# Kernel optimization log

Hardware: AMD Instinct MI355X
Metric: run time of the kernel (lower is better)

Reference implementation:

```python
import jax, jax.numpy as jnp
import numpy as np

# SRM neuron constants (match init_kwargs)
THRESH = 0.3
TAU_M = 16.0
TAU_S = 4.0
DT = 1.0
LENS = 0.5
DECAY_M = float(np.exp(-DT / TAU_M))
DECAY_S = float(np.exp(-DT / TAU_S))

B, T = 16, 16
SHAPES = [(B, 64, 64, 64), (B, 128, 64, 64), (B, 128, 32, 32), (B, 512), (B, 11)]


@jax.custom_vjp
def spike_fn(u):
    # Heaviside spike with rectangular surrogate gradient (width 2*lens),
    # the smooth-math stand-in for the LUT-based grad_u_approx.
    return (u > THRESH).astype(u.dtype)

def _spike_fwd(u):
    return spike_fn(u), u

def _spike_bwd(u, g):
    surr = (jnp.abs(u - THRESH) < LENS).astype(u.dtype) / (2.0 * LENS)
    return (g * surr,)

spike_fn.defvjp(_spike_fwd, _spike_bwd)


def conv(x, w):
    # 3x3 conv, stride 1, padding 1, no bias (NCHW / OIHW)
    return jax.lax.conv_general_dilated(x, w, (1, 1), [(1, 1), (1, 1)],
                                        dimension_numbers=('NCHW', 'OIHW', 'NCHW'))


def maxpool2(x):
    return jax.lax.reduce_window(x, -jnp.inf, jax.lax.max, (1, 1, 2, 2), (1, 1, 2, 2), 'VALID')


def srm_update(I, vm, vs, s_prev):
    # SRM dynamics: two exponential traces (LUT exp decay in original),
    # reset via previous spike, membrane potential u = vm - vs.
    vm = DECAY_M * vm * (1.0 - s_prev) + I
    vs = DECAY_S * vs * (1.0 - s_prev) + I
    s = spike_fn(vm - vs)
    return vm, vs, s


def _xavier(key, shape):
    if len(shape) == 4:  # OIHW conv
        fan_in = shape[1] * shape[2] * shape[3]
        fan_out = shape[0] * shape[2] * shape[3]
    else:  # Linear [out, in]
        fan_in, fan_out = shape[1], shape[0]
    lim = float(np.sqrt(6.0 / (fan_in + fan_out)))
    return jax.random.uniform(key, shape, jnp.float32, -lim, lim)


def setup_inputs() -> dict:
    key = jax.random.key(0)
    ks = jax.random.split(key, 6)
    inp = jax.random.uniform(ks[0], (B, T, 2, 64, 64), jnp.float32)
    return {
        'input': inp,
        'W0': _xavier(ks[1], (64, 2, 3, 3)),
        'W1': _xavier(ks[2], (128, 64, 3, 3)),
        'W2': _xavier(ks[3], (128, 128, 3, 3)),
        'W3': _xavier(ks[4], (512, 32768)),
        'W4': _xavier(ks[5], (11, 512)),
        'batch_size': B,
        'num_steps': T,
    }


def reference(input, W0, W1, W2, W3, W4, batch_size, num_steps):
    x = jnp.transpose(input, (1, 0, 2, 3, 4))  # [T, B, 2, 64, 64]
    z = lambda s: jnp.zeros(s, jnp.float32)
    vm = tuple(z(s) for s in SHAPES)
    vs = tuple(z(s) for s in SHAPES)
    sp = tuple(z(s) for s in SHAPES)
    out_sum = z((batch_size, 11))

    def step(carry, xt):
        vm, vs, sp, out_sum = carry
        in_spike = jnp.clip(xt, 0.0, 1.0)  # limit == 'yes'
        vm0, vs0, s0 = srm_update(conv(in_spike, W0), vm[0], vs[0], sp[0])
        vm1, vs1, s1 = srm_update(conv(s0, W1), vm[1], vs[1], sp[1])
        p1 = maxpool2(s1)                                    # [B,128,32,32]
        vm2, vs2, s2 = srm_update(conv(p1, W2), vm[2], vs[2], sp[2])
        p2 = maxpool2(s2).reshape(batch_size, -1)            # [B, 32768]
        vm3, vs3, s3 = srm_update(p2 @ W3.T, vm[3], vs[3], sp[3])
        vm4, vs4, s4 = srm_update(s3 @ W4.T, vm[4], vs[4], sp[4])
        new_carry = ((vm0, vm1, vm2, vm3, vm4), (vs0, vs1, vs2, vs3, vs4),
                     (s0, s1, s2, s3, s4), out_sum + s4)
        return new_carry, None

    (_, _, _, out_sum), _ = jax.lax.scan(step, (vm, vs, sp, out_sum), x)
    return out_sum / num_steps
```

## Files before the change

kernel.cpp:

```cpp
#include <hip/hip_runtime.h>
#include <hip/hip_bf16.h>
#include <math.h>

#define DM 0.9394130628134758f
#define DSC 0.7788007830714049f
#define TH 0.3f

#define B 16
#define T 16

typedef short short8 __attribute__((ext_vector_type(8)));
typedef float f32x4 __attribute__((ext_vector_type(4)));
typedef int i32x4 __attribute__((ext_vector_type(4)));

__device__ __forceinline__ void srm(float& m, float& s, float p, float I, float& spk) {
    m = DM * m * (1.f - p) + I;
    s = DSC * s * (1.f - p) + I;
    spk = (m - s > TH) ? 1.f : 0.f;
}

__global__ __launch_bounds__(256) void k_prep_i8(const float* __restrict__ W,
                                                 signed char* __restrict__ Wd,
                                                 int CO, int CI,
                                                 float s1, float s2, float s3) {
    int idx = blockIdx.x * 256 + threadIdx.x;
    int total = CO * CI * 9;
    if (idx >= total) return;
    int tap = idx % 9, tmp = idx / 9, ci = tmp % CI, co = tmp / CI;
    float w = W[((size_t)co * CI + ci) * 9 + tap];
    float d1 = rintf(w / s1);
    float r1 = fmaf(-d1, s1, w);
    float d2 = rintf(r1 / s2);
    float r2 = fmaf(-d2, s2, r1);
    float d3 = rintf(r2 / s3);
    d1 = fminf(fmaxf(d1, -127.f), 127.f);
    d2 = fminf(fmaxf(d2, -127.f), 127.f);
    d3 = fminf(fmaxf(d3, -127.f), 127.f);
    size_t base = ((size_t)tap * CO + co) * CI + ci;
    size_t stride = (size_t)9 * CO * CI;
    Wd[base] = (signed char)(int)d1;
    Wd[base + stride] = (signed char)(int)d2;
    Wd[base + 2 * stride] = (signed char)(int)d3;
}

__global__ __launch_bounds__(256) void k_prep3(const float* __restrict__ W3,
                                               unsigned short* __restrict__ W3p) {
    int bid = blockIdx.x;
    int ot = bid >> 8, ks4 = bid & 255;
    int lane = threadIdx.x & 63, wv = threadIdx.x >> 6;
    int kstep = ks4 * 4 + wv;
    int n = lane & 15, q = lane >> 4;
    const float* src = W3 + (size_t)(ot * 16 + n) * 32768 + kstep * 32 + q * 8;
    float4 w0 = *(const float4*)src;
    float4 w1 = *(const float4*)(src + 4);
    float wj[8] = {w0.x, w0.y, w0.z, w0.w, w1.x, w1.y, w1.z, w1.w};
    short8 hh, mm, ll;
#pragma unroll
    for (int j = 0; j < 8; j++) {
        __hip_bfloat16 h = __float2bfloat16(wj[j]);
        float hf = __bfloat162float(h);
        __hip_bfloat16 m = __float2bfloat16(wj[j] - hf);
        float mf = __bfloat162float(m);
        __hip_bfloat16 l = __float2bfloat16(wj[j] - hf - mf);
        hh[j] = *(short*)&h; mm[j] = *(short*)&m; ll[j] = *(short*)&l;
    }
    size_t pos = (((size_t)ot * 1024 + kstep) * 64 + lane) * 8;
    *(short8*)(W3p + pos) = hh;
    *(short8*)(W3p + 16777216 + pos) = mm;
    *(short8*)(W3p + 33554432 + pos) = ll;
}

#define S0T 20
__global__ __launch_bounds__(256) void k_conv0T(const float* __restrict__ in,
                                                const float* __restrict__ W0,
                                                signed char* __restrict__ s0b) {
    __shared__ float tile[2][10][S0T];
    int bid = blockIdx.x;
    int b = bid & 15;
    int rest = bid >> 4;
    int xt = rest & 3, yt = rest >> 2;
    int tid = threadIdx.x;
    int cog = tid & 7, pxg = tid >> 3;
    int y0 = yt * 8, x0 = xt * 16;

    float m[8][4] = {}, s[8][4] = {};
    unsigned pmask = 0;

    const float* wb = W0 + (size_t)cog * 8 * 2 * 9;

    for (int t = 0; t < T; t++) {
        if (t) __syncthreads();
        for (int i = tid; i < 360; i += 256) {
            int ci = i / 180, rem = i - ci * 180;
            int r = rem / 18, cc = rem - r * 18;
            int gy = y0 + r - 1, gx = x0 + cc - 1;
            float v = 0.f;
            if ((unsigned)gy < 64u && (unsigned)gx < 64u) {
                const float* src = in + ((size_t)((b * T + t) * 2 + ci)) * 4096;
                v = fminf(fmaxf(src[gy * 64 + gx], 0.f), 1.f);
            }
            tile[ci][r][cc] = v;
        }
        __syncthreads();

        float acc[8][4] = {};
#pragma unroll
        for (int ci = 0; ci < 2; ci++) {
#pragma unroll
            for (int dy = 0; dy < 3; dy++) {
#pragma unroll
                for (int dx = 0; dx < 3; dx++) {
                    float wv[8];
#pragma unroll
                    for (int c = 0; c < 8; c++)
                        wv[c] = wb[((size_t)c * 2 + ci) * 9 + dy * 3 + dx];
#pragma unroll
                    for (int j = 0; j < 4; j++) {
                        int px = pxg + 32 * j;
                        int y = px >> 4, x = px & 15;
                        float tv = tile[ci][y + dy][x + dx];
#pragma unroll
                        for (int c = 0; c < 8; c++)
                            acc[c][j] += wv[c] * tv;
                    }
                }
            }
        }

        unsigned newmask = 0;
        signed char* s0p = s0b + ((size_t)(t * 16 + b) * 4096) * 64;
#pragma unroll
        for (int j = 0; j < 4; j++) {
            unsigned long long vv = 0ULL;
#pragma unroll
            for (int c = 0; c < 8; c++) {
                int bit = c * 4 + j;
                float p = (pmask >> bit) & 1 ? 1.f : 0.f;
                float spk;
                srm(m[c][j], s[c][j], p, acc[c][j], spk);
                bool on = spk > 0.5f;
                if (on) { newmask |= 1u << bit; vv |= 1ULL << (8 * c); }
            }
            int px = pxg + 32 * j;
            int gpx = (y0 + (px >> 4)) * 64 + x0 + (px & 15);
            *(unsigned long long*)(s0p + (size_t)gpx * 64 + cog * 8) = vv;
        }
        pmask = newmask;
    }
}

__global__ __launch_bounds__(512, 2) void k_conv1T(const signed char* __restrict__ s0b,
                                                   const signed char* __restrict__ W1d,
                                                   signed char* __restrict__ p1b,
                                                   float s1, float s2, float s3) {
    __shared__ i32x4 atile[1360];
    __shared__ i32x4 wlds[3456];
    int bid = blockIdx.x;
    int b = bid & 15;
    int rest = bid >> 4;
    int cg = rest & 3;
    int xh = (rest >> 2) & 1;
    int yq = rest >> 3;
    int tid = threadIdx.x;
    int lane = tid & 63, wv = tid >> 6;
    int cog_l = wv >> 2, rq = wv & 3;
    int n = lane & 15, q = lane >> 4;
    int y0 = yq * 8;

    const i32x4 zf = {0, 0, 0, 0};
    for (int i = tid; i < 1360; i += 512) atile[i] = zf;
    for (int idx = tid; idx < 3456; idx += 512) {
        int qq = idx & 3, nn = (idx >> 2) & 15;
        int r27 = (idx >> 6) % 27, cl = idx / 1728;
        int tm = r27 % 3, tap = r27 / 3;
        int dst = (idx & ~3) | ((qq + (nn >> 1)) & 3);
        wlds[dst] = *(const i32x4*)(W1d +
            ((size_t)(tm * 9 + tap) * 128 + cg * 32 + cl * 16 + nn) * 64 + qq * 16);
    }

    int off_[3], ldsi_[3];
    bool ok_[3];
#pragma unroll
    for (int j = 0; j < 3; j++) {
        ok_[j] = false; ldsi_[j] = 0; off_[j] = 0;
        int item = tid + j * 512;
        if (item < 1360) {
            int r = item / 136, rem = item - r * 136;
            int xl = rem >> 2, c = rem & 3;
            ldsi_[j] = (r * 34 + xl) * 4 + ((c + (xl >> 1)) & 3);
            int gy = y0 - 1 + r;
            int gx = xh * 32 + xl - 1;
            if ((unsigned)gy < 64u && (unsigned)gx < 64u) {
                ok_[j] = true;
                off_[j] = (gy * 64 + gx) * 64 + c * 16;
            }
        }
    }
    __syncthreads();

    {
        const signed char* sb = s0b + ((size_t)(0 * 16 + b) * 4096) * 64;
#pragma unroll
        for (int j = 0; j < 3; j++)
            if (ok_[j]) atile[ldsi_[j]] = *(const i32x4*)(sb + off_[j]);
    }
    __syncthreads();

    int xp_s = lane >> 2, cq = lane & 3;
    int xt_s = xp_s >> 3, q_s = (xp_s >> 1) & 3, rp_s = xp_s & 1;

    int cbase_w = cog_l * 1728;
    float sm[4][4] = {}, ss[4][4] = {};
    unsigned pmask = 0;

    for (int t = 0; t < T; t++) {
        i32x4 pf0 = zf, pf1 = zf, pf2 = zf;
        bool pfv = (t + 1 < T);
        if (pfv) {
            const signed char* sb1 = s0b + ((size_t)((t + 1) * 16 + b) * 4096) * 64;
            if (ok_[0]) pf0 = *(const i32x4*)(sb1 + off_[0]);
            if (ok_[1]) pf1 = *(const i32x4*)(sb1 + off_[1]);
            if (ok_[2]) pf2 = *(const i32x4*)(sb1 + off_[2]);
        }

        i32x4 accH[4], accM[4], accL[4];
#pragma unroll
        for (int u = 0; u < 4; u++) { accH[u] = zf; accM[u] = zf; accL[u] = zf; }

#pragma unroll
        for (int dy = 0; dy < 3; dy++) {
#pragma unroll
            for (int dx = 0; dx < 3; dx++) {
                int tap = dy * 3 + dx;
                i32x4 Af[2][2];
#pragma unroll
                for (int ro = 0; ro < 2; ro++) {
                    int r = rq * 2 + ro + dy;
#pragma unroll
                    for (int xt = 0; xt < 2; xt++) {
                        int x = xt * 16 + n + dx;
                        Af[ro][xt] = atile[(r * 34 + x) * 4 + ((q + (x >> 1)) & 3)];
                    }
                }
                {
                    i32x4 Bf = wlds[cbase_w + (tap * 3 + 0) * 64 + n * 4 + ((q + (n >> 1)) & 3)];
#pragma unroll
                    for (int ro = 0; ro < 2; ro++)
#pragma unroll
                        for (int xt = 0; xt < 2; xt++)
                            accH[ro * 2 + xt] = __builtin_amdgcn_mfma_i32_16x16x64_i8(
                                Af[ro][xt], Bf, accH[ro * 2 + xt], 0, 0, 0);
                }
                {
                    i32x4 Bf = wlds[cbase_w + (tap * 3 + 1) * 64 + n * 4 + ((q + (n >> 1)) & 3)];
#pragma unroll
                    for (int ro = 0; ro < 2; ro++)
#pragma unroll
                        for (int xt = 0; xt < 2; xt++)
                            accM[ro * 2 + xt] = __builtin_amdgcn_mfma_i32_16x16x64_i8(
                                Af[ro][xt], Bf, accM[ro * 2 + xt], 0, 0, 0);
                }
                {
                    i32x4 Bf = wlds[cbase_w + (tap * 3 + 2) * 64 + n * 4 + ((q + (n >> 1)) & 3)];
#pragma unroll
                    for (int ro = 0; ro < 2; ro++)
#pragma unroll
                        for (int xt = 0; xt < 2; xt++)
                            accL[ro * 2 + xt] = __builtin_amdgcn_mfma_i32_16x16x64_i8(
                                Af[ro][xt], Bf, accL[ro * 2 + xt], 0, 0, 0);
                }
            }
        }

        unsigned newmask = 0;
#pragma unroll
        for (int ro = 0; ro < 2; ro++)
#pragma unroll
            for (int xt = 0; xt < 2; xt++)
#pragma unroll
                for (int r = 0; r < 4; r++) {
                    int u = ro * 2 + xt;
                    int bit = u * 4 + r;
                    float p = (pmask >> bit) & 1 ? 1.f : 0.f;
                    float I = fmaf((float)accH[u][r], s1,
                             fmaf((float)accM[u][r], s2, (float)accL[u][r] * s3));
                    float spk;
                    srm(sm[u][r], ss[u][r], p, I, spk);
                    if (spk > 0.5f) newmask |= 1u << bit;
                }
        pmask = newmask;

        unsigned bits4 = 0;
#pragma unroll
        for (int xt = 0; xt < 2; xt++)
#pragma unroll
            for (int rp = 0; rp < 2; rp++) {
                int i0 = (0 * 2 + xt) * 4 + 2 * rp;
                int i1 = (1 * 2 + xt) * 4 + 2 * rp;
                unsigned on = ((newmask >> i0) | (newmask >> (i0 + 1)) |
                               (newmask >> i1) | (newmask >> (i1 + 1))) & 1u;
                unsigned long long bal = __ballot(on != 0);
                if (xt == xt_s && rp == rp_s)
                    bits4 = (unsigned)(bal >> (q_s * 16 + cq * 4)) & 0xFu;
            }
        unsigned vv = (bits4 & 1u) | (((bits4 >> 1) & 1u) << 8) |
                      (((bits4 >> 2) & 1u) << 16) | (((bits4 >> 3) & 1u) << 24);
        signed char* pb = p1b + (((size_t)(t * 16 + b) * 8) + cg * 2 + cog_l) * 16384;
        int px = (yq * 4 + rq) * 32 + xh * 16 + xp_s;
        *(unsigned*)(pb + (size_t)px * 16 + cq * 4) = vv;

        __syncthreads();
        if (pfv) {
            if (ok_[0]) atile[ldsi_[0]] = pf0;
            if (ok_[1]) atile[ldsi_[1]] = pf1;
            if (ok_[2]) atile[ldsi_[2]] = pf2;
        }
        __syncthreads();
    }
}

__global__ __launch_bounds__(512, 2) void k_conv2T(const signed char* __restrict__ p1b,
                                                   const signed char* __restrict__ W2d,
                                                   unsigned short* __restrict__ p2a,
                                                   float s1, float s2, float s3) {
    __shared__ i32x4 atile[4896];
    __shared__ i32x4 wlds[3456];
    int bid = blockIdx.x;
    int xcd = bid & 7, rest = bid >> 3;
    int b = ((rest & 1) << 3) | xcd;
    int yh = (rest >> 1) & 1;
    int cog = (rest >> 2) & 7;
    int tid = threadIdx.x;
    int lane = tid & 63, wv = tid >> 6;
    int n = lane & 15, q = lane >> 4;
    int y0 = yh * 16;

    const i32x4 zf = {0, 0, 0, 0};
    for (int i = tid; i < 4896; i += 512) atile[i] = zf;
    for (int idx = tid; idx < 3456; idx += 512) {
        int c8 = idx & 7, nn = (idx >> 3) & 15, rem = idx >> 7;
        int tm = rem % 3, tap = rem / 3;
        int dst = (idx & ~7) | (c8 ^ ((nn & 1) << 2));
        wlds[dst] = *(const i32x4*)(W2d +
            ((size_t)(tm * 9 + tap) * 128 + cog * 16 + nn) * 128 + c8 * 16);
    }

    int yr = yh * 8 + wv;
    int co = cog * 16 + n;

    float sm[2][2][4] = {}, ss[2][2][4] = {};
    unsigned pmask = 0;

    for (int t = 0; t < T; t++) {
        __syncthreads();
        const signed char* sb = p1b + (((size_t)(t * 16 + b)) << 17);
        for (int i = tid; i < 4608; i += 512) {
            int c = i & 7, x32 = (i >> 3) & 31, r = i >> 8;
            int gy = y0 - 1 + r;
            if ((unsigned)gy < 32u) {
                int xtile = x32 + 1;
                atile[(r * 34 + xtile) * 8 + (c ^ ((xtile & 1) << 2))] =
                    *(const i32x4*)(sb + (((size_t)c) << 14) + ((size_t)(gy * 32 + x32)) * 16);
            }
        }
        __syncthreads();

        i32x4 accH[2][2], accM[2][2], accL[2][2];
#pragma unroll
        for (int i = 0; i < 2; i++)
#pragma unroll
            for (int j = 0; j < 2; j++) { accH[i][j] = zf; accM[i][j] = zf; accL[i][j] = zf; }

#pragma unroll
        for (int ks = 0; ks < 2; ks++) {
#pragma unroll
            for (int dy = 0; dy < 3; dy++) {
                int rA = wv * 2 + dy, rB = rA + 1;
#pragma unroll
                for (int dx = 0; dx < 3; dx++) {
                    int tap = dy * 3 + dx;
                    i32x4 AfA[2], AfB[2];
#pragma unroll
                    for (int xt = 0; xt < 2; xt++) {
                        int x = xt * 16 + n + dx;
                        int slA = (ks * 4 + q) ^ ((x & 1) << 2);
                        AfA[xt] = atile[(rA * 34 + x) * 8 + slA];
                        AfB[xt] = atile[(rB * 34 + x) * 8 + slA];
                    }
                    int slB = (ks * 4 + q) ^ ((n & 1) << 2);
                    {
                        i32x4 Bf = wlds[(tap * 3 + 0) * 128 + n * 8 + slB];
#pragma unroll
                        for (int xt = 0; xt < 2; xt++) {
                            accH[0][xt] = __builtin_amdgcn_mfma_i32_16x16x64_i8(AfA[xt], Bf, accH[0][xt], 0, 0, 0);
                            accH[1][xt] = __builtin_amdgcn_mfma_i32_16x16x64_i8(AfB[xt], Bf, accH[1][xt], 0, 0, 0);
                        }
                    }
                    {
                        i32x4 Bf = wlds[(tap * 3 + 1) * 128 + n * 8 + slB];
#pragma unroll
                        for (int xt = 0; xt < 2; xt++) {
                            accM[0][xt] = __builtin_amdgcn_mfma_i32_16x16x64_i8(AfA[xt], Bf, accM[0][xt], 0, 0, 0);
                            accM[1][xt] = __builtin_amdgcn_mfma_i32_16x16x64_i8(AfB[xt], Bf, accM[1][xt], 0, 0, 0);
                        }
                    }
                    {
                        i32x4 Bf = wlds[(tap * 3 + 2) * 128 + n * 8 + slB];
#pragma unroll
                        for (int xt = 0; xt < 2; xt++) {
                            accL[0][xt] = __builtin_amdgcn_mfma_i32_16x16x64_i8(AfA[xt], Bf, accL[0][xt], 0, 0, 0);
                            accL[1][xt] = __builtin_amdgcn_mfma_i32_16x16x64_i8(AfB[xt], Bf, accL[1][xt], 0, 0, 0);
                        }
                    }
                }
            }
        }

        unsigned newmask = 0;
#pragma unroll
        for (int yo = 0; yo < 2; yo++)
#pragma unroll
            for (int xt = 0; xt < 2; xt++)
#pragma unroll
                for (int r = 0; r < 4; r++) {
                    int bit = (yo * 2 + xt) * 4 + r;
                    float p = (pmask >> bit) & 1 ? 1.f : 0.f;
                    float I = fmaf((float)accH[yo][xt][r], s1,
                             fmaf((float)accM[yo][xt][r], s2, (float)accL[yo][xt][r] * s3));
                    float spk;
                    srm(sm[yo][xt][r], ss[yo][xt][r], p, I, spk);
                    if (spk > 0.5f) newmask |= 1u << bit;
                }
        pmask = newmask;

        int kstep = co * 8 + (yr >> 1);
        size_t base_t = ((size_t)t * 1024 + kstep) * 512;
#pragma unroll
        for (int xt = 0; xt < 2; xt++) {
            int i00 = (0 * 2 + xt) * 4 + 0, i10 = (1 * 2 + xt) * 4 + 0;
            int i01 = (0 * 2 + xt) * 4 + 2, i11 = (1 * 2 + xt) * 4 + 2;
            unsigned on0 = ((newmask >> i00) | (newmask >> (i00 + 1)) |
                            (newmask >> i10) | (newmask >> (i10 + 1))) & 1u;
            unsigned on1 = ((newmask >> i01) | (newmask >> (i01 + 1)) |
                            (newmask >> i11) | (newmask >> (i11 + 1))) & 1u;
            unsigned v32 = (on0 ? 0x3F80u : 0u) | (on1 ? 0x3F800000u : 0u);
            int qp = (yr & 1) * 2 + xt;
            *(unsigned*)(p2a + base_t + (size_t)(qp * 16 + b) * 8 + q * 2) = v32;
        }
    }
}

__global__ __launch_bounds__(256) void k_fc3(const unsigned short* __restrict__ p2a,
                                             const unsigned short* __restrict__ W3p,
                                             float* __restrict__ I3p) {
    int bid = blockIdx.x;
    int ob = bid & 7, r2 = bid >> 3;
    int t = r2 & 15, ks = r2 >> 4;
    int lane = threadIdx.x & 63, w = threadIdx.x >> 6;
    int ot = ob * 4 + w;

    const unsigned short* ap = p2a + ((size_t)t * 1024 + ks * 128) * 512 + lane * 8;
    const unsigned short* bp = W3p + ((size_t)ot * 1024 + ks * 128) * 512 + lane * 8;

    f32x4 acc = {0.f, 0.f, 0.f, 0.f};
#pragma unroll 8
    for (int kk = 0; kk < 128; kk++) {
        short8 A = *(const short8*)(ap + (size_t)kk * 512);
        short8 B0 = *(const short8*)(bp + (size_t)kk * 512);
        short8 B1 = *(const short8*)(bp + 16777216 + (size_t)kk * 512);
        short8 B2 = *(const short8*)(bp + 33554432 + (size_t)kk * 512);
        acc = __builtin_amdgcn_mfma_f32_16x16x32_bf16(A, B0, acc, 0, 0, 0);
        acc = __builtin_amdgcn_mfma_f32_16x16x32_bf16(A, B1, acc, 0, 0, 0);
        acc = __builtin_amdgcn_mfma_f32_16x16x32_bf16(A, B2, acc, 0, 0, 0);
    }
    int n = lane & 15, q = lane >> 4;
    float* op = I3p + ((size_t)(t * 8 + ks)) * 8192 + ot * 16 + n;
#pragma unroll
    for (int r = 0; r < 4; r++)
        op[(size_t)(q * 4 + r) * 512] = acc[r];
}

__global__ __launch_bounds__(256) void k_srm3T(const float* __restrict__ I3p,
                                               float* __restrict__ sp3) {
    int idx = blockIdx.x * 256 + threadIdx.x;
    float m = 0.f, s = 0.f, p = 0.f;
    for (int t = 0; t < T; t++) {
        float I = 0.f;
#pragma unroll
        for (int ks = 0; ks < 8; ks++) I += I3p[((size_t)(t * 8 + ks)) * 8192 + idx];
        float spk;
        srm(m, s, p, I, spk);
        p = spk;
        sp3[t * 8192 + idx] = spk;
    }
}

__global__ __launch_bounds__(256) void k_fc4g(const float* __restrict__ sp3,
                                              const float* __restrict__ W4,
                                              float* __restrict__ I4) {
    int t = blockIdx.x, tid = threadIdx.x;
    if (tid >= 176) return;
    int b = tid / 11, o = tid - b * 11;
    const float4* a = (const float4*)(sp3 + (size_t)t * 8192 + b * 512);
    const float4* w = (const float4*)(W4 + o * 512);
    float acc = 0.f;
    for (int k = 0; k < 128; k++) {
        float4 x = a[k], y = w[k];
        acc += x.x * y.x + x.y * y.y + x.z * y.z + x.w * y.w;
    }
    I4[(size_t)(t * 16 + b) * 11 + o] = acc;
}

__global__ __launch_bounds__(256) void k_fc4s(const float* __restrict__ I4,
                                              float* __restrict__ out) {
    int tid = threadIdx.x;
    if (tid >= 176) return;
    int b = tid / 11, o = tid - b * 11;
    float m = 0.f, s = 0.f, p = 0.f, sum = 0.f;
    for (int t = 0; t < T; t++) {
        float I = I4[(size_t)(t * 16 + b) * 11 + o];
        float spk;
        srm(m, s, p, I, spk);
        p = spk;
        sum += spk;
    }
    out[tid] = sum * 0.0625f;
}

extern "C" void kernel_launch(void* const* d_in, const int* in_sizes, int n_in,
                              void* d_out, int out_size, void* d_ws, size_t ws_size,
                              hipStream_t stream) {
    const float* in = (const float*)d_in[0];
    const float* W0 = (const float*)d_in[1];
    const float* W1 = (const float*)d_in[2];
    const float* W2 = (const float*)d_in[3];
    const float* W3 = (const float*)d_in[4];
    const float* W4 = (const float*)d_in[5];
    float* out = (float*)d_out;
    char* ws = (char*)d_ws;

    size_t off = 0;
    auto alloc = [&](size_t bytes) {
        void* p = ws + off;
        off += (bytes + 255) & ~(size_t)255;
        return p;
    };
    signed char* s0b = (signed char*)alloc((size_t)256 * 4096 * 64);
    signed char* p1b = (signed char*)alloc((size_t)256 * 1024 * 128);
    unsigned short* p2a = (unsigned short*)alloc((size_t)16 * 1024 * 512 * 2);
    float* I3p = (float*)alloc((size_t)128 * 8192 * 4);
    float* sp3 = (float*)alloc((size_t)16 * 8192 * 4);
    float* I4  = (float*)alloc((size_t)256 * 11 * 4);
    signed char* W1d = (signed char*)alloc((size_t)3 * 9 * 128 * 64);
    signed char* W2d = (signed char*)alloc((size_t)3 * 9 * 128 * 128);
    unsigned short* W3p = (unsigned short*)alloc((size_t)3 * 512 * 32768 * 2);

    double lim1 = sqrt(6.0 / (64.0 * 9 + 128.0 * 9));
    double lim2 = sqrt(6.0 / (128.0 * 9 + 128.0 * 9));
    float s1a = (float)(lim1 / 127.0);
    float s2a = s1a / 254.0f;
    float s3a = s2a / 64.0f;
    float s1b = (float)(lim2 / 127.0);
    float s2b = s1b / 254.0f;
    float s3b = s2b / 64.0f;

    k_prep_i8<<<(9 * 128 * 64 + 255) / 256, 256, 0, stream>>>(W1, W1d, 128, 64, s1a, s2a, s3a);
    k_prep_i8<<<(9 * 128 * 128 + 255) / 256, 256, 0, stream>>>(W2, W2d, 128, 128, s1b, s2b, s3b);
    k_prep3<<<8192, 256, 0, stream>>>(W3, W3p);

    k_conv0T<<<512, 256, 0, stream>>>(in, W0, s0b);
    k_conv1T<<<1024, 512, 0, stream>>>(s0b, W1d, p1b, s1a, s2a, s3a);
    k_conv2T<<<256, 512, 0, stream>>>(p1b, W2d, p2a, s1b, s2b, s3b);
    k_fc3<<<1024, 256, 0, stream>>>(p2a, W3p, I3p);
    k_srm3T<<<8192 / 256, 256, 0, stream>>>(I3p, sp3);
    k_fc4g<<<16, 256, 0, stream>>>(sp3, W4, I4);
    k_fc4s<<<1, 256, 0, stream>>>(I4, out);
}
```

Before: 662.1 us.

## Retile conv1 blocks to full-width rows with one output-channel group each

Each conv1 block now covers a full 64-pixel-wide strip of 8 rows for a single 16-channel output group, in place of a half-width strip for two groups. This shrinks the weight LDS by half, grows the activation tile, and raises the launch-bounds occupancy hint from 2 to 4 blocks per CU. The register prefetch of the next timestep's input is dropped in favour of a synchronous load at the top of each step. The aim is more resident waves to hide latency, at the cost of losing explicit load/compute overlap and reloading activations once per channel group.

```diff
diff --git a/kernel.cpp b/kernel.cpp
--- a/kernel.cpp
+++ b/kernel.cpp
@@ -149,79 +149,59 @@
     }
 }
 
-__global__ __launch_bounds__(512, 2) void k_conv1T(const signed char* __restrict__ s0b,
+__global__ __launch_bounds__(512, 4) void k_conv1T(const signed char* __restrict__ s0b,
                                                    const signed char* __restrict__ W1d,
                                                    signed char* __restrict__ p1b,
                                                    float s1, float s2, float s3) {
-    __shared__ i32x4 atile[1360];
-    __shared__ i32x4 wlds[3456];
+    __shared__ i32x4 atile[2640];
+    __shared__ i32x4 wlds[1728];
     int bid = blockIdx.x;
     int b = bid & 15;
     int rest = bid >> 4;
-    int cg = rest & 3;
-    int xh = (rest >> 2) & 1;
+    int cog = rest & 7;
     int yq = rest >> 3;
     int tid = threadIdx.x;
     int lane = tid & 63, wv = tid >> 6;
-    int cog_l = wv >> 2, rq = wv & 3;
+    int rq = wv & 3, xh = wv >> 2;
     int n = lane & 15, q = lane >> 4;
     int y0 = yq * 8;
 
     const i32x4 zf = {0, 0, 0, 0};
-    for (int i = tid; i < 1360; i += 512) atile[i] = zf;
-    for (int idx = tid; idx < 3456; idx += 512) {
+    for (int i = tid; i < 2640; i += 512) atile[i] = zf;
+    for (int idx = tid; idx < 1728; idx += 512) {
         int qq = idx & 3, nn = (idx >> 2) & 15;
-        int r27 = (idx >> 6) % 27, cl = idx / 1728;
+        int r27 = idx >> 6;
         int tm = r27 % 3, tap = r27 / 3;
         int dst = (idx & ~3) | ((qq + (nn >> 1)) & 3);
         wlds[dst] = *(const i32x4*)(W1d +
-            ((size_t)(tm * 9 + tap) * 128 + cg * 32 + cl * 16 + nn) * 64 + qq * 16);
-    }
-
-    int off_[3], ldsi_[3];
-    bool ok_[3];
-#pragma unroll
-    for (int j = 0; j < 3; j++) {
-        ok_[j] = false; ldsi_[j] = 0; off_[j] = 0;
+            ((size_t)(tm * 9 + tap) * 128 + cog * 16 + nn) * 64 + qq * 16);
+    }
+
+    int off_[5], ldsi_[5];
+#pragma unroll
+    for (int j = 0; j < 5; j++) {
         int item = tid + j * 512;
-        if (item < 1360) {
-            int r = item / 136, rem = item - r * 136;
-            int xl = rem >> 2, c = rem & 3;
-            ldsi_[j] = (r * 34 + xl) * 4 + ((c + (xl >> 1)) & 3);
-            int gy = y0 - 1 + r;
-            int gx = xh * 32 + xl - 1;
-            if ((unsigned)gy < 64u && (unsigned)gx < 64u) {
-                ok_[j] = true;
-                off_[j] = (gy * 64 + gx) * 64 + c * 16;
-            }
-        }
-    }
-    __syncthreads();
-
-    {
-        const signed char* sb = s0b + ((size_t)(0 * 16 + b) * 4096) * 64;
-#pragma unroll
-        for (int j = 0; j < 3; j++)
-            if (ok_[j]) atile[ldsi_[j]] = *(const i32x4*)(sb + off_[j]);
+        int c = item & 3, x64 = (item >> 2) & 63, r = item >> 8;
+        int xl = x64 + 1;
+        ldsi_[j] = (r * 66 + xl) * 4 + ((c + (xl >> 1)) & 3);
+        int gy = y0 - 1 + r;
+        off_[j] = ((unsigned)gy < 64u) ? ((gy * 64 + x64) * 64 + c * 16) : -1;
     }
     __syncthreads();
 
     int xp_s = lane >> 2, cq = lane & 3;
     int xt_s = xp_s >> 3, q_s = (xp_s >> 1) & 3, rp_s = xp_s & 1;
 
-    int cbase_w = cog_l * 1728;
     float sm[4][4] = {}, ss[4][4] = {};
     unsigned pmask = 0;
 
     for (int t = 0; t < T; t++) {
-        i32x4 pf0 = zf, pf1 = zf, pf2 = zf;
-        bool pfv = (t + 1 < T);
-        if (pfv) {
-            const signed char* sb1 = s0b + ((size_t)((t + 1) * 16 + b) * 4096) * 64;
-            if (ok_[0]) pf0 = *(const i32x4*)(sb1 + off_[0]);
-            if (ok_[1]) pf1 = *(const i32x4*)(sb1 + off_[1]);
-            if (ok_[2]) pf2 = *(const i32x4*)(sb1 + off_[2]);
-        }
+        if (t) __syncthreads();
+        const signed char* sb = s0b + ((size_t)(t * 16 + b) * 4096) * 64;
+#pragma unroll
+        for (int j = 0; j < 5; j++)
+            if (off_[j] >= 0) atile[ldsi_[j]] = *(const i32x4*)(sb + off_[j]);
+        __syncthreads();
 
         i32x4 accH[4], accM[4], accL[4];
 #pragma unroll
@@ -238,12 +218,13 @@
                     int r = rq * 2 + ro + dy;
 #pragma unroll
                     for (int xt = 0; xt < 2; xt++) {
-                        int x = xt * 16 + n + dx;
-                        Af[ro][xt] = atile[(r * 34 + x) * 4 + ((q + (x >> 1)) & 3)];
+                        int x = xh * 32 + xt * 16 + n + dx;
+                        Af[ro][xt] = atile[(r * 66 + x) * 4 + ((q + (x >> 1)) & 3)];
                     }
                 }
+                int wslot = ((q + (n >> 1)) & 3);
                 {
-                    i32x4 Bf = wlds[cbase_w + (tap * 3 + 0) * 64 + n * 4 + ((q + (n >> 1)) & 3)];
+                    i32x4 Bf = wlds[(tap * 3 + 0) * 64 + n * 4 + wslot];
 #pragma unroll
                     for (int ro = 0; ro < 2; ro++)
 #pragma unroll
@@ -252,7 +233,7 @@
                                 Af[ro][xt], Bf, accH[ro * 2 + xt], 0, 0, 0);
                 }
                 {
-                    i32x4 Bf = wlds[cbase_w + (tap * 3 + 1) * 64 + n * 4 + ((q + (n >> 1)) & 3)];
+                    i32x4 Bf = wlds[(tap * 3 + 1) * 64 + n * 4 + wslot];
 #pragma unroll
                     for (int ro = 0; ro < 2; ro++)
 #pragma unroll
@@ -261,7 +242,7 @@
                                 Af[ro][xt], Bf, accM[ro * 2 + xt], 0, 0, 0);
                 }
                 {
-                    i32x4 Bf = wlds[cbase_w + (tap * 3 + 2) * 64 + n * 4 + ((q + (n >> 1)) & 3)];
+                    i32x4 Bf = wlds[(tap * 3 + 2) * 64 + n * 4 + wslot];
 #pragma unroll
                     for (int ro = 0; ro < 2; ro++)
 #pragma unroll
@@ -305,17 +286,9 @@
             }
         unsigned vv = (bits4 & 1u) | (((bits4 >> 1) & 1u) << 8) |
                       (((bits4 >> 2) & 1u) << 16) | (((bits4 >> 3) & 1u) << 24);
-        signed char* pb = p1b + (((size_t)(t * 16 + b) * 8) + cg * 2 + cog_l) * 16384;
+        signed char* pb = p1b + (((size_t)(t * 16 + b) * 8) + cog) * 16384;
         int px = (yq * 4 + rq) * 32 + xh * 16 + xp_s;
         *(unsigned*)(pb + (size_t)px * 16 + cq * 4) = vv;
-
-        __syncthreads();
-        if (pfv) {
-            if (ok_[0]) atile[ldsi_[0]] = pf0;
-            if (ok_[1]) atile[ldsi_[1]] = pf1;
-            if (ok_[2]) atile[ldsi_[2]] = pf2;
-        }
-        __syncthreads();
     }
 }
 
```

Measured after the change: 784.3 us. 18.5% more time.
